# Kernel tuning notes

Hardware: AMD Instinct MI355X
Metric: run time of the kernel (lower is better)

The kernel has to match this reference:

```python
import jax, jax.numpy as jnp
import numpy as np

M, N, K = 4096, 8192, 4096


def setup_inputs() -> dict:
    key = jax.random.key(0)
    k1, k2, k3, k4 = jax.random.split(key, 4)
    a = jax.random.randint(k1, (M, K), 0, 127, dtype=jnp.int32)  # int8 activations
    b = jax.random.randint(k2, (N, K), 0, 127, dtype=jnp.int32)  # int8 weights (row-major [N,K])
    alpha_row = jax.random.uniform(k3, (M, 1), dtype=jnp.float16)  # per-row dequant scale
    alpha_col = jax.random.uniform(k4, (1, N), dtype=jnp.float16)  # per-col dequant scale
    return {"a": a, "b": b, "alpha_row": alpha_row, "alpha_col": alpha_col}


def reference(a, b, alpha_row, alpha_col):
    # x = a @ b.T in fp32 (int8 values upcast), then rescale by outer product of scales
    x = jnp.matmul(a.astype(jnp.float32), b.astype(jnp.float32).T)  # [M, N]
    scale = alpha_row.astype(jnp.float32) * alpha_col.astype(jnp.float32)  # [M, N] via broadcast
    out = x * scale
    return out.astype(jnp.float16)
```

## Files before the change

kernel.cpp:

```cpp
#include <hip/hip_runtime.h>
#include <cstdint>
#include <cstddef>

#define M_DIM 4096
#define N_DIM 8192
#define K_DIM 4096

typedef __attribute__((ext_vector_type(4))) int int4v;

__global__ void __launch_bounds__(256) pack_frag(const int* __restrict__ a,
                                                 const int* __restrict__ b,
                                                 unsigned char* __restrict__ pa,
                                                 unsigned char* __restrict__ pb) {
    size_t t = (size_t)blockIdx.x * 256 + threadIdx.x;
    const size_t NA = (size_t)(M_DIM / 16) * (K_DIM / 64) * 64;
    const int* __restrict__ src;
    unsigned char* __restrict__ dst;
    if (t < NA) {
        src = a; dst = pa;
    } else {
        src = b; dst = pb; t -= NA;
    }
    const int l = (int)(t & 63);
    const int s = (int)((t >> 6) & 63);
    const int p = (int)(t >> 12);
    const int* g = src + ((size_t)(16 * p + (l & 15))) * K_DIM + s * 64 + (l >> 4) * 16;
    const int4v* g4 = (const int4v*)g;
    int4v o;
#pragma unroll
    for (int q = 0; q < 4; ++q) {
        int4v v = g4[q];
        o[q] = (v[0] & 0xff) | ((v[1] & 0xff) << 8) | ((v[2] & 0xff) << 16) | (v[3] << 24);
    }
    ((int4v*)dst)[t] = o;
}

__device__ inline void async_copy16(const unsigned char* g, unsigned char* l) {
    __builtin_amdgcn_global_load_lds(
        (const __attribute__((address_space(1))) void*)g,
        (__attribute__((address_space(3))) void*)l,
        16, 0, 0);
}

__global__ void __launch_bounds__(512, 2) gemm_i8(const unsigned char* __restrict__ Ap,
                                                  const unsigned char* __restrict__ Bp,
                                                  const _Float16* __restrict__ arow,
                                                  const _Float16* __restrict__ acol,
                                                  _Float16* __restrict__ Cout) {
    __shared__ __align__(16) unsigned char As[2 * 16384];
    __shared__ __align__(16) unsigned char Bs[2 * 16384];

    const int tid  = threadIdx.x;
    const int lane = tid & 63;
    const int wave = tid >> 6;
    const int bn   = blockIdx.x;
    const int bm   = blockIdx.y;

    const int pm0 = (wave & 3) * 4;
    const int pn0 = (wave >> 2) * 8;

    const unsigned char* ag[2];
    const unsigned char* bg[2];
    int slo[2];
#pragma unroll
    for (int r = 0; r < 2; ++r) {
        const int p = 2 * wave + r;
        ag[r]  = Ap + ((size_t)(bm * 16 + p) * 64) * 1024 + lane * 16;
        bg[r]  = Bp + ((size_t)(bn * 16 + p) * 64) * 1024 + lane * 16;
        slo[r] = p * 1024;
    }

    const int a_off = pm0 * 1024 + lane * 16;
    const int b_off = pn0 * 1024 + lane * 16;

    int4v acc[4][8];
#pragma unroll
    for (int i = 0; i < 4; ++i)
#pragma unroll
        for (int j = 0; j < 8; ++j) acc[i][j] = (int4v)0;

    const int NT = K_DIM / 64;

#pragma unroll
    for (int r = 0; r < 2; ++r) {
        async_copy16(ag[r], As + slo[r]);
        async_copy16(bg[r], Bs + slo[r]);
    }
    __syncthreads();

#pragma unroll 2
    for (int T = 0; T < NT; ++T) {
        const int cur = (T & 1) * 16384;
        const int nxt = cur ^ 16384;

        if (T + 1 < NT) {
            const size_t gko = (size_t)(T + 1) * 1024;
#pragma unroll
            for (int r = 0; r < 2; ++r) {
                async_copy16(ag[r] + gko, As + nxt + slo[r]);
                async_copy16(bg[r] + gko, Bs + nxt + slo[r]);
            }
        }

        int4v af[4], bf[8];
#pragma unroll
        for (int i = 0; i < 4; ++i)
            af[i] = *(const int4v*)(As + cur + a_off + i * 1024);
#pragma unroll
        for (int j = 0; j < 8; ++j)
            bf[j] = *(const int4v*)(Bs + cur + b_off + j * 1024);

#pragma unroll
        for (int i = 0; i < 4; ++i)
#pragma unroll
            for (int j = 0; j < 8; ++j)
                acc[i][j] = __builtin_amdgcn_mfma_i32_16x16x64_i8(af[i], bf[j],
                                                                  acc[i][j], 0, 0, 0);

        __syncthreads();
    }

    const int gcol0 = bn * 256 + pn0 * 16 + (lane & 15);
    float ac8[8];
#pragma unroll
    for (int j = 0; j < 8; ++j) ac8[j] = (float)acol[gcol0 + j * 16];

    const size_t grow0 = (size_t)bm * 256 + pm0 * 16 + (lane >> 4) * 4;
#pragma unroll
    for (int i = 0; i < 4; ++i) {
#pragma unroll
        for (int r = 0; r < 4; ++r) {
            const size_t row = grow0 + i * 16 + r;
            const float ar = (float)arow[row];
            _Float16* outp = Cout + row * (size_t)N_DIM + gcol0;
#pragma unroll
            for (int j = 0; j < 8; ++j) {
                float v = (float)acc[i][j][r] * ar * ac8[j];
                outp[j * 16] = (_Float16)v;
            }
        }
    }
}

extern "C" void kernel_launch(void* const* d_in, const int* in_sizes, int n_in,
                              void* d_out, int out_size, void* d_ws, size_t ws_size,
                              hipStream_t stream) {
    const int* a = (const int*)d_in[0];
    const int* b = (const int*)d_in[1];
    const _Float16* ar = (const _Float16*)d_in[2];
    const _Float16* ac = (const _Float16*)d_in[3];
    _Float16* out = (_Float16*)d_out;

    unsigned char* pa = (unsigned char*)d_ws;
    unsigned char* pb = pa + (size_t)M_DIM * K_DIM;

    const size_t total_frag = (size_t)(M_DIM / 16 + N_DIM / 16) * (K_DIM / 64) * 64;
    pack_frag<<<(int)(total_frag / 256), 256, 0, stream>>>(a, b, pa, pb);

    dim3 grid(N_DIM / 256, M_DIM / 256);
    gemm_i8<<<grid, 512, 0, stream>>>(pa, pb, ar, ac, out);
}
```

Baseline: 382.4 us.

## Process two K-tiles per iteration with four-stage LDS ring buffer

```diff
diff --git a/kernel.cpp b/kernel.cpp
--- a/kernel.cpp
+++ b/kernel.cpp
@@ -47,8 +47,8 @@
                                                   const _Float16* __restrict__ arow,
                                                   const _Float16* __restrict__ acol,
                                                   _Float16* __restrict__ Cout) {
-    __shared__ __align__(16) unsigned char As[2 * 16384];
-    __shared__ __align__(16) unsigned char Bs[2 * 16384];
+    __shared__ __align__(16) unsigned char As[4 * 16384];
+    __shared__ __align__(16) unsigned char Bs[4 * 16384];
 
     const int tid  = threadIdx.x;
     const int lane = tid & 63;
@@ -65,8 +65,8 @@
 #pragma unroll
     for (int r = 0; r < 2; ++r) {
         const int p = 2 * wave + r;
-        ag[r]  = Ap + ((size_t)(bm * 16 + p) * 64) * 1024 + lane * 16;
-        bg[r]  = Bp + ((size_t)(bn * 16 + p) * 64) * 1024 + lane * 16;
+        ag[r]  = Ap + (size_t)(bm * 16 + p) * 65536 + lane * 16;
+        bg[r]  = Bp + (size_t)(bn * 16 + p) * 65536 + lane * 16;
         slo[r] = p * 1024;
     }
 
@@ -85,37 +85,50 @@
     for (int r = 0; r < 2; ++r) {
         async_copy16(ag[r], As + slo[r]);
         async_copy16(bg[r], Bs + slo[r]);
+        async_copy16(ag[r] + 1024, As + 16384 + slo[r]);
+        async_copy16(bg[r] + 1024, Bs + 16384 + slo[r]);
     }
     __syncthreads();
 
-#pragma unroll 2
-    for (int T = 0; T < NT; ++T) {
-        const int cur = (T & 1) * 16384;
-        const int nxt = cur ^ 16384;
-
-        if (T + 1 < NT) {
-            const size_t gko = (size_t)(T + 1) * 1024;
+    for (int T = 0; T < NT; T += 2) {
+        if (T + 2 < NT) {
+            const size_t gko = (size_t)(T + 2) * 1024;
+            const int buf = ((T + 2) & 3) * 16384;
 #pragma unroll
             for (int r = 0; r < 2; ++r) {
-                async_copy16(ag[r] + gko, As + nxt + slo[r]);
-                async_copy16(bg[r] + gko, Bs + nxt + slo[r]);
+                async_copy16(ag[r] + gko, As + buf + slo[r]);
+                async_copy16(bg[r] + gko, Bs + buf + slo[r]);
+            }
+            const size_t gko3 = gko + 1024;
+            const int buf3 = ((T + 3) & 3) * 16384;
+#pragma unroll
+            for (int r = 0; r < 2; ++r) {
+                async_copy16(ag[r] + gko3, As + buf3 + slo[r]);
+                async_copy16(bg[r] + gko3, Bs + buf3 + slo[r]);
             }
         }
 
-        int4v af[4], bf[8];
 #pragma unroll
-        for (int i = 0; i < 4; ++i)
-            af[i] = *(const int4v*)(As + cur + a_off + i * 1024);
+        for (int u = 0; u < 2; ++u) {
+            const int cur = ((T + u) & 3) * 16384;
+            const unsigned char* Ac = As + cur;
+            const unsigned char* Bc = Bs + cur;
+
+            int4v af[4], bf[8];
 #pragma unroll
-        for (int j = 0; j < 8; ++j)
-            bf[j] = *(const int4v*)(Bs + cur + b_off + j * 1024);
+            for (int i = 0; i < 4; ++i)
+                af[i] = *(const int4v*)(Ac + a_off + i * 1024);
+#pragma unroll
+            for (int j = 0; j < 8; ++j)
+                bf[j] = *(const int4v*)(Bc + b_off + j * 1024);
 
 #pragma unroll
-        for (int i = 0; i < 4; ++i)
+            for (int i = 0; i < 4; ++i)
 #pragma unroll
-            for (int j = 0; j < 8; ++j)
-                acc[i][j] = __builtin_amdgcn_mfma_i32_16x16x64_i8(af[i], bf[j],
-                                                                  acc[i][j], 0, 0, 0);
+                for (int j = 0; j < 8; ++j)
+                    acc[i][j] = __builtin_amdgcn_mfma_i32_16x16x64_i8(af[i], bf[j],
+                                                                      acc[i][j], 0, 0, 0);
+        }
 
         __syncthreads();
     }
```

Result: faster. 374.0 us (-2.2%).
